# Performance work log

Measured on AMD Instinct MI355X. Metric: run time of the kernel, lower is better.

Reference implementation:

```python
import jax, jax.numpy as jnp
import numpy as np

N_NODES = 50000
N_EDGES = 800000
HEADS = 6
LEAKY = 0.2


def gat_layer(x, W, a_src, a_dst, src, dst):
    """Multi-head GAT layer (Velickovic et al.), concat heads + ELU.
    x: [N, F_in], W: [H, F_in, F_out], a_src/a_dst: [H, F_out]."""
    n = x.shape[0]
    h = jnp.einsum('nf,hfo->nho', x, W)              # [N, H, F_out]
    es = jnp.einsum('nho,ho->nh', h, a_src)          # source attention term
    ed = jnp.einsum('nho,ho->nh', h, a_dst)          # destination attention term
    e = jax.nn.leaky_relu(es[src] + ed[dst], LEAKY)  # [E, H] per-edge logits
    # segment softmax over incoming edges of each destination node
    emax = jax.ops.segment_max(e, dst, num_segments=n)
    emax = jnp.where(jnp.isfinite(emax), emax, jnp.zeros_like(emax))
    ex = jnp.exp(e - emax[dst])                      # [E, H]
    denom = jax.ops.segment_sum(ex, dst, num_segments=n)
    alpha = ex / (denom[dst] + 1e-16)                # [E, H]
    msg = alpha[:, :, None] * h[src]                 # [E, H, F_out]
    out = jax.ops.segment_sum(msg, dst, num_segments=n)  # [N, H, F_out]
    return jax.nn.elu(out).reshape(n, -1)            # concat heads


def setup_inputs() -> dict:
    key = jax.random.key(0)
    ks = jax.random.split(key, 16)
    glorot = lambda k, shape: jax.random.normal(k, shape, jnp.float32) * np.sqrt(2.0 / (shape[-2] + shape[-1]))
    inp = {
        'x': jax.random.normal(ks[0], (N_NODES, 11), jnp.float32),
        'edge_index': jax.random.randint(ks[1], (2, N_EDGES), 0, N_NODES, jnp.int32),
        'W1': glorot(ks[2], (HEADS, 11, 16)),
        'a1s': glorot(ks[3], (HEADS, 16)),
        'a1d': glorot(ks[4], (HEADS, 16)),
        'W2': glorot(ks[5], (HEADS, 96, 32)),
        'a2s': glorot(ks[6], (HEADS, 32)),
        'a2d': glorot(ks[7], (HEADS, 32)),
        'W3': glorot(ks[8], (HEADS, 192, 64)),
        'a3s': glorot(ks[9], (HEADS, 64)),
        'a3d': glorot(ks[10], (HEADS, 64)),
        'Wd': glorot(ks[11], (384, 1)),
        'bd': jnp.zeros((1,), jnp.float32),
    }
    return inp


def reference(x, edge_index, W1, a1s, a1d, W2, a2s, a2d, W3, a3s, a3d, Wd, bd):
    src, dst = edge_index[0], edge_index[1]
    h = gat_layer(x, W1, a1s, a1d, src, dst)   # [N, 96]
    h = gat_layer(h, W2, a2s, a2d, src, dst)   # [N, 192]
    h = gat_layer(h, W3, a3s, a3d, src, dst)   # [N, 384]
    g = jnp.sum(h, axis=0).reshape(1, -1)      # sum pool -> [1, 384]
    g = g / jnp.maximum(jnp.linalg.norm(g, axis=1, keepdims=True), 1e-12)  # F.normalize
    out = g @ Wd + bd                          # Dense 384->1, linear nonlin
    return jnp.squeeze(out, 1)                 # [1]
```

## Files before the change

### kernel.cpp

```cpp
#include <hip/hip_runtime.h>
#include <hip/hip_bf16.h>


#define HHEADS 6

typedef __attribute__((ext_vector_type(8))) short bf16x8;
typedef __attribute__((ext_vector_type(4))) float f32x4;
typedef __attribute__((ext_vector_type(2))) float f32x2;

typedef __attribute__((address_space(3))) unsigned int lds_uint;
typedef const __attribute__((address_space(1))) unsigned int glb_uint;

__device__ __forceinline__ float bfl(unsigned u) { return __uint_as_float(u << 16); }
__device__ __forceinline__ float bfh(unsigned u) { return __uint_as_float(u & 0xffff0000u); }
__device__ __forceinline__ unsigned short f2bf(float v) {
    unsigned u = __float_as_uint(v);
    return (unsigned short)((u + 0x7fffu + ((u >> 16) & 1u)) >> 16);
}
__device__ __forceinline__ float bf2f(unsigned short h) {
    return __uint_as_float((unsigned)h << 16);
}
__device__ __forceinline__ unsigned fkey(float f) {
    unsigned u = __float_as_uint(f);
    return (u >> 31) ? ~u : (u | 0x80000000u);
}
__device__ __forceinline__ float funkey(unsigned k) {
    return (k >> 31) ? __uint_as_float(k & 0x7fffffffu) : __uint_as_float(~k);
}

__device__ __forceinline__ void xpose4(float& v0, float& v1, float& v2, float& v3, int b) {
    bool hi = (b & 2) != 0;
    float s0 = hi ? v0 : v2;
    float s1 = hi ? v1 : v3;
    s0 = __shfl_xor(s0, 2, 64);
    s1 = __shfl_xor(s1, 2, 64);
    v0 = hi ? s0 : v0;
    v1 = hi ? s1 : v1;
    v2 = hi ? v2 : s0;
    v3 = hi ? v3 : s1;
    bool od = (b & 1) != 0;
    float t0 = od ? v0 : v1;
    t0 = __shfl_xor(t0, 1, 64);
    v0 = od ? t0 : v0;
    v1 = od ? v1 : t0;
    float t1 = od ? v2 : v3;
    t1 = __shfl_xor(t1, 1, 64);
    v2 = od ? t1 : v2;
    v3 = od ? v3 : t1;
}

__global__ void zero_misc(int* __restrict__ count, int* __restrict__ cursor,
                          float* __restrict__ g, unsigned* __restrict__ gmax,
                          unsigned short* __restrict__ apH,
                          long pad3_off, long pad3_cnt, long pad6_off, long pad6_cnt, int n) {
    long i = (long)blockIdx.x * blockDim.x + threadIdx.x;
    long stride = (long)gridDim.x * blockDim.x;
    for (long j = i; j < n; j += stride) {
        count[j] = 0;
        cursor[j] = 0;
    }
    if (i < 384) g[i] = 0.f;
    if (i < 12) gmax[i] = 0u;
    for (long j = i; j < pad3_cnt; j += stride) apH[pad3_off + j] = 0;
    for (long j = i; j < pad6_cnt; j += stride) apH[pad6_off + j] = 0;
}

__global__ void hist_kernel(const int* __restrict__ dst, int* __restrict__ count, int E) {
    int e = blockIdx.x * blockDim.x + threadIdx.x;
    if (e >= E) return;
    atomicAdd(&count[dst[e]], 1);
}

__global__ void scan_block(const int* __restrict__ count, int* __restrict__ offsets,
                           int* __restrict__ bsum, int n) {
    __shared__ int s[1024];
    int i = blockIdx.x * 1024 + threadIdx.x;
    int v = (i < n) ? count[i] : 0;
    s[threadIdx.x] = v;
    __syncthreads();
    for (int off = 1; off < 1024; off <<= 1) {
        int t = (threadIdx.x >= (unsigned)off) ? s[threadIdx.x - off] : 0;
        __syncthreads();
        s[threadIdx.x] += t;
        __syncthreads();
    }
    if (i < n) offsets[i] = s[threadIdx.x] - v;
    if (threadIdx.x == 1023) bsum[blockIdx.x] = s[1023];
}

__global__ void scan_tops(int* __restrict__ bsum, int nb) {
    __shared__ int s[64];
    int t = threadIdx.x;
    int v = (t < nb) ? bsum[t] : 0;
    s[t] = v;
    __syncthreads();
    for (int off = 1; off < 64; off <<= 1) {
        int tmp = (t >= off) ? s[t - off] : 0;
        __syncthreads();
        s[t] += tmp;
        __syncthreads();
    }
    if (t < nb) bsum[t] = s[t] - v;
}

__global__ void scan_add(int* __restrict__ offsets, const int* __restrict__ bsum, int n,
                         int total) {
    int i = blockIdx.x * 1024 + threadIdx.x;
    if (i < n) offsets[i] += bsum[blockIdx.x];
    if (i == 0) offsets[n] = total;
}

__global__ void scatter_kernel(const int* __restrict__ src, const int* __restrict__ dst,
                               const int* __restrict__ offsets, int* __restrict__ cursor,
                               int* __restrict__ ssrc, int E) {
    int e = blockIdx.x * blockDim.x + threadIdx.x;
    if (e >= E) return;
    int d = dst[e];
    int pos = offsets[d] + atomicAdd(&cursor[d], 1);
    ssrc[pos] = src[e];
}

__global__ void repack_w(const float* __restrict__ W, float* __restrict__ Wp, int FIN, int F) {
    int HF = HHEADS * F;
    int i = blockIdx.x * blockDim.x + threadIdx.x;
    if (i >= FIN * HF) return;
    int k = i / HF, c = i % HF;
    int hd = c / F, f = c % F;
    Wp[i] = W[(hd * FIN + k) * F + f];
}

__global__ void repack_w_mfma(const float* __restrict__ W, unsigned short* __restrict__ bh,
                              int FIN, int F, int NPAD) {
    int i = blockIdx.x * blockDim.x + threadIdx.x;
    if (i >= FIN * NPAD) return;
    int k = i / NPAD, n = i % NPAD;
    int NKT = FIN / 32;
    int HF = HHEADS * F;
    float w = 0.f;
    if (n < HF) {
        int hd = n / F, f = n % F;
        w = W[(hd * FIN + k) * F + f];
    }
    size_t e = ((size_t)((n >> 4) * NKT + (k >> 5)) * 64 + ((n & 15) | (((k >> 3) & 3) << 4))) * 8 +
               (k & 7);
    bh[e] = f2bf(w);
}

template <int BM, int BN, int BK>
__global__ __launch_bounds__(256) void gemm_small_attn(const float* __restrict__ A,
                                                       const float* __restrict__ B,
                                                       unsigned char* __restrict__ C8,
                                                       const float* __restrict__ as_,
                                                       const float* __restrict__ ad_,
                                                       float* __restrict__ es,
                                                       float* __restrict__ ed, int M, int K,
                                                       int N) {
    __shared__ float As[BK][BM + 4];
    __shared__ float Bs[BK][BN];
    int tid = threadIdx.x;
    int tx = tid % 16, ty = tid / 16;
    int m0 = blockIdx.y * BM, n0 = blockIdx.x * BN;
    float acc[4][4] = {};
    for (int kk0 = 0; kk0 < K; kk0 += BK) {
#pragma unroll
        for (int i = 0; i < (BM * BK) / 256; ++i) {
            int idx = tid + i * 256;
            int m = idx / BK, k = idx % BK;
            float v = 0.f;
            if (m0 + m < M && kk0 + k < K) v = A[(size_t)(m0 + m) * K + kk0 + k];
            As[k][m] = v;
        }
#pragma unroll
        for (int i = 0; i < (BK * BN) / 1024; ++i) {
            int idx = tid + i * 256;
            int k = idx / (BN / 4), n4 = idx % (BN / 4);
            float4 v = make_float4(0.f, 0.f, 0.f, 0.f);
            if (kk0 + k < K && n0 + n4 * 4 < N)
                v = *(const float4*)&B[(size_t)(kk0 + k) * N + n0 + n4 * 4];
            *(float4*)&Bs[k][n4 * 4] = v;
        }
        __syncthreads();
#pragma unroll
        for (int k = 0; k < BK; ++k) {
            float4 av = *(const float4*)&As[k][ty * 4];
            float4 bv = *(const float4*)&Bs[k][tx * 4];
            float a[4] = {av.x, av.y, av.z, av.w};
            float b[4] = {bv.x, bv.y, bv.z, bv.w};
#pragma unroll
            for (int i = 0; i < 4; ++i)
#pragma unroll
                for (int j = 0; j < 4; ++j) acc[i][j] += a[i] * b[j];
        }
        __syncthreads();
    }
    bool colok = (n0 + tx * 4) < N;
    float asv[4], adv[4];
#pragma unroll
    for (int j = 0; j < 4; ++j) {
        int col = n0 + tx * 4 + j;
        asv[j] = (col < N) ? as_[col] : 0.f;
        adv[j] = (col < N) ? ad_[col] : 0.f;
    }
#pragma unroll
    for (int i = 0; i < 4; ++i) {
        int m = m0 + ty * 4 + i;
        bool mok = m < M;
        if (mok && colok) {
            int pk = __builtin_amdgcn_cvt_pk_fp8_f32(acc[i][0], acc[i][1], 0, false);
            pk = __builtin_amdgcn_cvt_pk_fp8_f32(acc[i][2], acc[i][3], pk, true);
            *(unsigned*)&C8[(size_t)m * N + n0 + tx * 4] = (unsigned)pk;
        }
        float ps = 0.f, pd = 0.f;
#pragma unroll
        for (int j = 0; j < 4; ++j) {
            ps += acc[i][j] * asv[j];
            pd += acc[i][j] * adv[j];
        }
        ps += __shfl_down(ps, 2, 4);
        ps += __shfl_down(ps, 1, 4);
        pd += __shfl_down(pd, 2, 4);
        pd += __shfl_down(pd, 1, 4);
        if (mok && colok && (tx & 3) == 0) {
            int hd = (n0 + tx * 4) >> 4;
            es[(size_t)m * HHEADS + hd] = ps;
            ed[(size_t)m * HHEADS + hd] = pd;
        }
    }
}

template <int K, int NREAL, int NPAD, int F, int MT>
__global__ __launch_bounds__(256) void gemm_attn_mfma(
    const unsigned short* __restrict__ Ah, const unsigned short* __restrict__ Bh,
    unsigned char* __restrict__ C8, const float* __restrict__ as_,
    const float* __restrict__ ad_, float* __restrict__ es, float* __restrict__ ed,
    unsigned* __restrict__ gmax, int M) {
    constexpr int NKT = K / 32;
    __shared__ unsigned short sB[NKT * 4096];
    __shared__ unsigned short sA[2][4096];
    int tid = threadIdx.x;
    int lane = tid & 63, wave = tid >> 6;
    int wrow = wave >> 1, wcol = wave & 1;
    int quad = lane >> 4, c16 = lane & 15;

    int nwg = gridDim.x * gridDim.y;
    int hh = blockIdx.y * gridDim.x + blockIdx.x;
    int q = nwg >> 3, r = nwg & 7;
    int xcd = hh & 7, pos = hh >> 3;
    int wk = (xcd < r ? xcd * (q + 1) : r * (q + 1) + (xcd - r) * q) + pos;
    int bx = wk % gridDim.x, by = wk / gridDim.x;

    int n0 = bx * 128;
    int bn16 = n0 >> 4;
    int nmt = (M + 127) >> 7;

#pragma unroll
    for (int kt2 = 0; kt2 < NKT; ++kt2) {
#pragma unroll
        for (int rep = 0; rep < 2; ++rep) {
            int chunk = tid + rep * 256;
            int tile = chunk >> 6, e8 = chunk & 63;
            size_t boff = ((size_t)((bn16 + tile) * NKT + kt2) * 64 + e8) * 8;
            __builtin_amdgcn_global_load_lds((glb_uint*)&Bh[boff],
                                             (lds_uint*)&sB[kt2 * 4096 + chunk * 8], 16, 0, 0);
        }
    }
    auto STAGE_A = [&](int mti, int kt2, int buf) {
#pragma unroll
        for (int rep = 0; rep < 2; ++rep) {
            int chunk = tid + rep * 256;
            int tile = chunk >> 6, e8 = chunk & 63;
            size_t aoff = ((size_t)((mti * 8 + tile) * NKT + kt2) * 64 + e8) * 8;
            __builtin_amdgcn_global_load_lds((glb_uint*)&Ah[aoff],
                                             (lds_uint*)&sA[buf][chunk * 8], 16, 0, 0);
        }
    };
    STAGE_A(min(by * MT, nmt - 1), 0, 0);
    asm volatile("s_waitcnt vmcnt(0)" ::: "memory");
    __builtin_amdgcn_s_barrier();

    float asv[4], adv[4];
#pragma unroll
    for (int j = 0; j < 4; ++j) {
        int col = n0 + wcol * 64 + j * 16 + c16;
        bool ok = col < NREAL;
        asv[j] = ok ? as_[col] : 0.f;
        adv[j] = ok ? ad_[col] : 0.f;
    }
    float mx = -1e30f;
    float mxA = -1e30f, mxB = -1e30f;
    bool colvalid = (n0 + wcol * 64) < NREAL;
    int b4 = lane & 3;

    f32x4 acc[4][4] = {};
    const int T = MT * NKT;
    int mt = 0, kt = 0;
    for (int t = 0; t < T; ++t) {
        int cur = t & 1;
        int nkt = kt + 1, nmt2 = mt;
        if (nkt == NKT) {
            nkt = 0;
            nmt2 = mt + 1;
        }
        if (t + 1 < T) STAGE_A(min(by * MT + nmt2, nmt - 1), nkt, cur ^ 1);
        bf16x8 fah[4], fbh[4];
#pragma unroll
        for (int i = 0; i < 4; ++i) {
            fah[i] = *(const bf16x8*)&sA[cur][(wrow * 4 + i) * 512 + lane * 8];
            fbh[i] = *(const bf16x8*)&sB[kt * 4096 + (wcol * 4 + i) * 512 + lane * 8];
        }
        asm volatile("s_waitcnt lgkmcnt(0)" ::: "memory");
        __builtin_amdgcn_sched_barrier(0);
#pragma unroll
        for (int i = 0; i < 4; ++i)
#pragma unroll
            for (int j = 0; j < 4; ++j)
                acc[i][j] = __builtin_amdgcn_mfma_f32_16x16x32_bf16(fah[i], fbh[j], acc[i][j],
                                                                    0, 0, 0);
        if (kt == NKT - 1) {
            int m0 = (by * MT + mt) * 128;
            if (m0 < M) {
#pragma unroll
                for (int i = 0; i < 4; ++i) {
#pragma unroll
                    for (int r2 = 0; r2 < 4; ++r2) {
                        int m = m0 + wrow * 64 + i * 16 + quad * 4 + r2;
                        bool mok = m < M;
                        if (F == 64) {
                            float ps = acc[i][0][r2] * asv[0] + acc[i][1][r2] * asv[1] +
                                       acc[i][2][r2] * asv[2] + acc[i][3][r2] * asv[3];
                            float pd = acc[i][0][r2] * adv[0] + acc[i][1][r2] * adv[1] +
                                       acc[i][2][r2] * adv[2] + acc[i][3][r2] * adv[3];
#pragma unroll
                            for (int off = 8; off > 0; off >>= 1) {
                                ps += __shfl_down(ps, off, 16);
                                pd += __shfl_down(pd, off, 16);
                            }
                            if (mok && c16 == 0) {
                                int hd = (n0 + wcol * 64) / 64;
                                es[(size_t)m * HHEADS + hd] = ps;
                                ed[(size_t)m * HHEADS + hd] = pd;
                                mx = fmaxf(mx, ps);
                            }
                        } else {
                            float psA = acc[i][0][r2] * asv[0] + acc[i][1][r2] * asv[1];
                            float pdA = acc[i][0][r2] * adv[0] + acc[i][1][r2] * adv[1];
                            float psB = acc[i][2][r2] * asv[2] + acc[i][3][r2] * asv[3];
                            float pdB = acc[i][2][r2] * adv[2] + acc[i][3][r2] * adv[3];
#pragma unroll
                            for (int off = 8; off > 0; off >>= 1) {
                                psA += __shfl_down(psA, off, 16);
                                pdA += __shfl_down(pdA, off, 16);
                                psB += __shfl_down(psB, off, 16);
                                pdB += __shfl_down(pdB, off, 16);
                            }
                            if (mok && c16 == 0 && colvalid) {
                                int colbase = n0 + wcol * 64;
                                int hd = colbase / 32;
                                es[(size_t)m * HHEADS + hd] = psA;
                                ed[(size_t)m * HHEADS + hd] = pdA;
                                es[(size_t)m * HHEADS + hd + 1] = psB;
                                ed[(size_t)m * HHEADS + hd + 1] = pdB;
                                mxA = fmaxf(mxA, psA);
                                mxB = fmaxf(mxB, psB);
                            }
                        }
                    }
                }
#pragma unroll
                for (int i = 0; i < 4; ++i) {
                    int m = m0 + wrow * 64 + i * 16 + quad * 4 + b4;
                    bool mok = m < M;
#pragma unroll
                    for (int j = 0; j < 4; ++j) {
                        float v0 = acc[i][j][0], v1 = acc[i][j][1], v2 = acc[i][j][2],
                              v3 = acc[i][j][3];
                        xpose4(v0, v1, v2, v3, b4);
                        int colb = n0 + wcol * 64 + j * 16 + (c16 & 12);
                        if (mok && (F == 64 || colvalid)) {
                            int pk = __builtin_amdgcn_cvt_pk_fp8_f32(v0, v1, 0, false);
                            pk = __builtin_amdgcn_cvt_pk_fp8_f32(v2, v3, pk, true);
                            *(unsigned*)&C8[(size_t)m * NREAL + colb] = (unsigned)pk;
                        }
                    }
                }
            }
#pragma unroll
            for (int i = 0; i < 4; ++i)
#pragma unroll
                for (int j = 0; j < 4; ++j) acc[i][j] = (f32x4){0.f, 0.f, 0.f, 0.f};
        }
        asm volatile("s_waitcnt vmcnt(0)" ::: "memory");
        __builtin_amdgcn_s_barrier();
        kt = nkt;
        mt = nmt2;
    }

    if (F == 64) {
#pragma unroll
        for (int off = 32; off > 0; off >>= 1) mx = fmaxf(mx, __shfl_xor(mx, off));
        if (lane == 0) atomicMax(&gmax[(n0 + wcol * 64) / 64], fkey(mx));
    } else {
        mxA = fmaxf(mxA, __shfl_xor(mxA, 16));
        mxA = fmaxf(mxA, __shfl_xor(mxA, 32));
        mxB = fmaxf(mxB, __shfl_xor(mxB, 16));
        mxB = fmaxf(mxB, __shfl_xor(mxB, 32));
        if (lane == 0 && colvalid) {
            int hd = (n0 + wcol * 64) / 32;
            atomicMax(&gmax[6 + hd], fkey(mxA));
            atomicMax(&gmax[6 + hd + 1], fkey(mxB));
        }
    }
}

template <int F>
__global__ __launch_bounds__(256) void aggregate_fused(
    const unsigned char* __restrict__ h8, const float* __restrict__ es,
    const float* __restrict__ ed, const int* __restrict__ offsets,
    const int* __restrict__ ssrc, unsigned short* __restrict__ oh, int n) {
    constexpr int HF = HHEADS * F;
    constexpr int C8 = HF / 8;
    int tid = blockIdx.x * blockDim.x + threadIdx.x;
    if (tid >= n * C8) return;
    int node = tid / C8, q = tid % C8;
    int c = q * 8, hd = c / F;
    int a = offsets[node], b = offsets[node + 1];
    float edv = ed[node * HHEADS + hd];
    float m = -1e30f, l = 0.f;
    float acc[8] = {};
    for (int j = a; j < b; ++j) {
        int s = ssrc[j];
        float v = es[s * HHEADS + hd] + edv;
        v = v > 0.f ? v : 0.2f * v;
        float mn = fmaxf(m, v);
        float r = __expf(m - mn);
        float wgt = __expf(v - mn);
        uint2 hv = *(const uint2*)&h8[(size_t)s * HF + c];
        f32x2 p0 = __builtin_amdgcn_cvt_pk_f32_fp8((int)hv.x, false);
        f32x2 p1 = __builtin_amdgcn_cvt_pk_f32_fp8((int)hv.x, true);
        f32x2 p2 = __builtin_amdgcn_cvt_pk_f32_fp8((int)hv.y, false);
        f32x2 p3 = __builtin_amdgcn_cvt_pk_f32_fp8((int)hv.y, true);
        l = l * r + wgt;
        acc[0] = acc[0] * r + wgt * p0[0];
        acc[1] = acc[1] * r + wgt * p0[1];
        acc[2] = acc[2] * r + wgt * p1[0];
        acc[3] = acc[3] * r + wgt * p1[1];
        acc[4] = acc[4] * r + wgt * p2[0];
        acc[5] = acc[5] * r + wgt * p2[1];
        acc[6] = acc[6] * r + wgt * p3[0];
        acc[7] = acc[7] * r + wgt * p3[1];
        m = mn;
    }
    float invd = 1.0f / (l + 1e-16f);
    unsigned short th[8];
#pragma unroll
    for (int k = 0; k < 8; ++k) {
        float v = acc[k] * invd;
        v = v > 0.f ? v : (__expf(v) - 1.0f);
        th[k] = f2bf(v);
    }
    constexpr int NKT = HF / 32;
    int lq = (node & 15) | (((c >> 3) & 3) << 4);
    size_t base = ((size_t)((node >> 4) * NKT + (c >> 5)) * 64 + lq) * 8;
    *(uint4*)&oh[base] = *(uint4*)th;
}

__global__ __launch_bounds__(256) void aggregate_wpn2(
    const unsigned char* __restrict__ h8, const float* __restrict__ es,
    const float* __restrict__ ed, const unsigned* __restrict__ gmax,
    const int* __restrict__ offsets, const int* __restrict__ ssrc,
    unsigned short* __restrict__ oh, int n) {
    constexpr int HF = 192;
    int wid = (int)((blockIdx.x * (unsigned)blockDim.x + threadIdx.x) >> 6);
    int lane = threadIdx.x & 63;
    if (wid >= n || lane >= 48) return;
    int node = wid;
    int hd = lane >> 3;
    int c = lane * 4;
    int a = offsets[node], b = offsets[node + 1];
    float edv = ed[node * HHEADS + hd];
    float mv = funkey(gmax[6 + hd]) + edv;
    float m = mv > 0.f ? mv : 0.2f * mv;
    float l = 0.f;
    float acc[4] = {};
    const unsigned char* hbase = h8 + c;
    int j = a;
    for (; j + 1 < b; j += 2) {
        int s0 = ssrc[j], s1 = ssrc[j + 1];
        float ev0 = es[(size_t)s0 * HHEADS + hd];
        float ev1 = es[(size_t)s1 * HHEADS + hd];
        unsigned h0 = *(const unsigned*)(hbase + (size_t)s0 * HF);
        unsigned h1 = *(const unsigned*)(hbase + (size_t)s1 * HF);
        float v0 = ev0 + edv;
        v0 = v0 > 0.f ? v0 : 0.2f * v0;
        float v1 = ev1 + edv;
        v1 = v1 > 0.f ? v1 : 0.2f * v1;
        float w0 = __expf(v0 - m);
        float w1 = __expf(v1 - m);
        {
            f32x2 p0 = __builtin_amdgcn_cvt_pk_f32_fp8((int)h0, false);
            f32x2 p1 = __builtin_amdgcn_cvt_pk_f32_fp8((int)h0, true);
            l += w0;
            acc[0] += w0 * p0[0];
            acc[1] += w0 * p0[1];
            acc[2] += w0 * p1[0];
            acc[3] += w0 * p1[1];
        }
        {
            f32x2 p0 = __builtin_amdgcn_cvt_pk_f32_fp8((int)h1, false);
            f32x2 p1 = __builtin_amdgcn_cvt_pk_f32_fp8((int)h1, true);
            l += w1;
            acc[0] += w1 * p0[0];
            acc[1] += w1 * p0[1];
            acc[2] += w1 * p1[0];
            acc[3] += w1 * p1[1];
        }
    }
    if (j < b) {
        int s0 = ssrc[j];
        float ev0 = es[(size_t)s0 * HHEADS + hd];
        unsigned h0 = *(const unsigned*)(hbase + (size_t)s0 * HF);
        float v0 = ev0 + edv;
        v0 = v0 > 0.f ? v0 : 0.2f * v0;
        float w0 = __expf(v0 - m);
        f32x2 p0 = __builtin_amdgcn_cvt_pk_f32_fp8((int)h0, false);
        f32x2 p1 = __builtin_amdgcn_cvt_pk_f32_fp8((int)h0, true);
        l += w0;
        acc[0] += w0 * p0[0];
        acc[1] += w0 * p0[1];
        acc[2] += w0 * p1[0];
        acc[3] += w0 * p1[1];
    }
    float invd = 1.0f / (l + 1e-16f);
    unsigned short th[4];
#pragma unroll
    for (int k = 0; k < 4; ++k) {
        float v = acc[k] * invd;
        v = v > 0.f ? v : (__expf(v) - 1.0f);
        th[k] = f2bf(v);
    }
    int lq = (node & 15) | (((c >> 3) & 3) << 4);
    size_t base = ((size_t)((node >> 4) * (HF / 32) + (c >> 5)) * 64 + lq) * 8 + (c & 7);
    *(uint2*)&oh[base] = *(uint2*)th;
}

__global__ __launch_bounds__(256) void aggregate_wpn3(
    const unsigned char* __restrict__ h8, const float* __restrict__ es,
    const float* __restrict__ ed, const unsigned* __restrict__ gmax,
    const int* __restrict__ offsets, const int* __restrict__ ssrc,
    __hip_bfloat16* __restrict__ outb, int n) {
    constexpr int HF = 384;
    int wid = (int)((blockIdx.x * (unsigned)blockDim.x + threadIdx.x) >> 6);
    int lane = threadIdx.x & 63;
    if (wid >= n || lane >= 48) return;
    int node = wid;
    int hd = lane >> 3;
    int c = lane * 8;
    int a = offsets[node], b = offsets[node + 1];
    float edv = ed[node * HHEADS + hd];
    float mv = funkey(gmax[hd]) + edv;
    float m = mv > 0.f ? mv : 0.2f * mv;
    float l = 0.f;
    float acc[8] = {};
    const unsigned char* hbase = h8 + c;
    int j = a;
    for (; j + 1 < b; j += 2) {
        int s0 = ssrc[j], s1 = ssrc[j + 1];
        float ev0 = es[(size_t)s0 * HHEADS + hd];
        float ev1 = es[(size_t)s1 * HHEADS + hd];
        uint2 h0 = *(const uint2*)(hbase + (size_t)s0 * HF);
        uint2 h1 = *(const uint2*)(hbase + (size_t)s1 * HF);
        float v0 = ev0 + edv;
        v0 = v0 > 0.f ? v0 : 0.2f * v0;
        float v1 = ev1 + edv;
        v1 = v1 > 0.f ? v1 : 0.2f * v1;
        float w0 = __expf(v0 - m);
        float w1 = __expf(v1 - m);
        {
            f32x2 p0 = __builtin_amdgcn_cvt_pk_f32_fp8((int)h0.x, false);
            f32x2 p1 = __builtin_amdgcn_cvt_pk_f32_fp8((int)h0.x, true);
            f32x2 p2 = __builtin_amdgcn_cvt_pk_f32_fp8((int)h0.y, false);
            f32x2 p3 = __builtin_amdgcn_cvt_pk_f32_fp8((int)h0.y, true);
            l += w0;
            acc[0] += w0 * p0[0];
            acc[1] += w0 * p0[1];
            acc[2] += w0 * p1[0];
            acc[3] += w0 * p1[1];
            acc[4] += w0 * p2[0];
            acc[5] += w0 * p2[1];
            acc[6] += w0 * p3[0];
            acc[7] += w0 * p3[1];
        }
        {
            f32x2 p0 = __builtin_amdgcn_cvt_pk_f32_fp8((int)h1.x, false);
            f32x2 p1 = __builtin_amdgcn_cvt_pk_f32_fp8((int)h1.x, true);
            f32x2 p2 = __builtin_amdgcn_cvt_pk_f32_fp8((int)h1.y, false);
            f32x2 p3 = __builtin_amdgcn_cvt_pk_f32_fp8((int)h1.y, true);
            l += w1;
            acc[0] += w1 * p0[0];
            acc[1] += w1 * p0[1];
            acc[2] += w1 * p1[0];
            acc[3] += w1 * p1[1];
            acc[4] += w1 * p2[0];
            acc[5] += w1 * p2[1];
            acc[6] += w1 * p3[0];
            acc[7] += w1 * p3[1];
        }
    }
    if (j < b) {
        int s0 = ssrc[j];
        float ev0 = es[(size_t)s0 * HHEADS + hd];
        uint2 h0 = *(const uint2*)(hbase + (size_t)s0 * HF);
        float v0 = ev0 + edv;
        v0 = v0 > 0.f ? v0 : 0.2f * v0;
        float w0 = __expf(v0 - m);
        f32x2 p0 = __builtin_amdgcn_cvt_pk_f32_fp8((int)h0.x, false);
        f32x2 p1 = __builtin_amdgcn_cvt_pk_f32_fp8((int)h0.x, true);
        f32x2 p2 = __builtin_amdgcn_cvt_pk_f32_fp8((int)h0.y, false);
        f32x2 p3 = __builtin_amdgcn_cvt_pk_f32_fp8((int)h0.y, true);
        l += w0;
        acc[0] += w0 * p0[0];
        acc[1] += w0 * p0[1];
        acc[2] += w0 * p1[0];
        acc[3] += w0 * p1[1];
        acc[4] += w0 * p2[0];
        acc[5] += w0 * p2[1];
        acc[6] += w0 * p3[0];
        acc[7] += w0 * p3[1];
    }
    float invd = 1.0f / (l + 1e-16f);
    __hip_bfloat16 tb[8];
#pragma unroll
    for (int k = 0; k < 8; ++k) {
        float v = acc[k] * invd;
        v = v > 0.f ? v : (__expf(v) - 1.0f);
        tb[k] = __float2bfloat16(v);
    }
    *(uint4*)&outb[(size_t)node * HF + c] = *(uint4*)tb;
}

__global__ void pool_kernel(const __hip_bfloat16* __restrict__ out3, float* __restrict__ g,
                            int n) {
    int b = blockIdx.x, t = threadIdx.x;
    int chunk = (n + gridDim.x - 1) / gridDim.x;
    int n0 = b * chunk, n1 = min(n, n0 + chunk);
    float a0 = 0.f, a1 = 0.f;
    const unsigned* p = (const unsigned*)out3;
    for (int node = n0; node < n1; ++node) {
        unsigned u = p[(size_t)node * 192 + t];
        a0 += bfl(u);
        a1 += bfh(u);
    }
    atomicAdd(&g[2 * t], a0);
    atomicAdd(&g[2 * t + 1], a1);
}

__global__ void final_kernel(const float* __restrict__ g, const float* __restrict__ Wd,
                             const float* __restrict__ bd, float* __restrict__ outp) {
    __shared__ float red[384];
    int t = threadIdx.x;
    float v = g[t];
    red[t] = v * v;
    __syncthreads();
    for (int s = 192; s >= 3; s >>= 1) {
        if (t < s) red[t] += red[t + s];
        __syncthreads();
    }
    __shared__ float scale_s;
    if (t == 0) {
        float norm = sqrtf(red[0] + red[1] + red[2]);
        scale_s = 1.0f / fmaxf(norm, 1e-12f);
    }
    __syncthreads();
    float scale = scale_s;
    red[t] = v * scale * Wd[t];
    __syncthreads();
    for (int s = 192; s >= 3; s >>= 1) {
        if (t < s) red[t] += red[t + s];
        __syncthreads();
    }
    if (t == 0) outp[0] = red[0] + red[1] + red[2] + bd[0];
}

extern "C" void kernel_launch(void* const* d_in, const int* in_sizes, int n_in, void* d_out,
                              int out_size, void* d_ws, size_t ws_size, hipStream_t stream) {
    const float* x = (const float*)d_in[0];
    const int* ei = (const int*)d_in[1];
    const float* W1 = (const float*)d_in[2];
    const float* a1s = (const float*)d_in[3];
    const float* a1d = (const float*)d_in[4];
    const float* W2 = (const float*)d_in[5];
    const float* a2s = (const float*)d_in[6];
    const float* a2d = (const float*)d_in[7];
    const float* W3 = (const float*)d_in[8];
    const float* a3s = (const float*)d_in[9];
    const float* a3d = (const float*)d_in[10];
    const float* Wd = (const float*)d_in[11];
    const float* bd = (const float*)d_in[12];
    float* outp = (float*)d_out;

    const int N = in_sizes[0] / 11;
    const int E = in_sizes[1] / 2;
    const int* src = ei;
    const int* dst = ei + E;

    const int NT16 = ((N + 127) / 128) * 8;
    const int NMT = (N + 127) / 128;

    char* w = (char*)d_ws;
    size_t off = 0;
    auto A = [&](size_t bytes) {
        size_t o = off;
        off += (bytes + 255) & ~(size_t)255;
        return o;
    };
    unsigned char* bufH = (unsigned char*)(w + A((size_t)N * 384 * 2));
    __hip_bfloat16* bufO = (__hip_bfloat16*)(w + A((size_t)N * 384 * 2));
    unsigned short* apH = (unsigned short*)(w + A((size_t)NT16 * 6 * 512 * 2));
    unsigned short* b2H = (unsigned short*)(w + A((size_t)16 * 3 * 512 * 2));
    unsigned short* b3H = (unsigned short*)(w + A((size_t)24 * 6 * 512 * 2));
    float* es = (float*)(w + A((size_t)N * HHEADS * 4));
    float* ed = (float*)(w + A((size_t)N * HHEADS * 4));
    unsigned* gmax = (unsigned*)(w + A(256));
    float* wp = (float*)(w + A((size_t)11 * 96 * 4));
    int* count = (int*)(w + A((size_t)(N + 1) * 4));
    int* cursor = (int*)(w + A((size_t)(N + 1) * 4));
    int* offsets = (int*)(w + A((size_t)(N + 1) * 4));
    int* bsum = (int*)(w + A(64 * 4));
    int* ssrc = (int*)(w + A((size_t)E * 4));
    float* g = (float*)(w + A(384 * 4));

    const long t16v = N / 16;
    const long padT = NT16 - t16v;
    zero_misc<<<(N + 255) / 256, 256, 0, stream>>>(count, cursor, g, gmax, apH,
                                                   t16v * 3 * 512, padT * 3 * 512,
                                                   t16v * 6 * 512, padT * 6 * 512, N);

    hist_kernel<<<(E + 255) / 256, 256, 0, stream>>>(dst, count, E);
    int nb = (N + 1023) / 1024;
    scan_block<<<nb, 1024, 0, stream>>>(count, offsets, bsum, N);
    scan_tops<<<1, 64, 0, stream>>>(bsum, nb);
    scan_add<<<nb, 1024, 0, stream>>>(offsets, bsum, N, E);
    scatter_kernel<<<(E + 255) / 256, 256, 0, stream>>>(src, dst, offsets, cursor, ssrc, E);

    repack_w<<<(11 * 96 + 255) / 256, 256, 0, stream>>>(W1, wp, 11, 16);
    repack_w_mfma<<<(96 * 256 + 255) / 256, 256, 0, stream>>>(W2, b2H, 96, 32, 256);
    repack_w_mfma<<<(192 * 384 + 255) / 256, 256, 0, stream>>>(W3, b3H, 192, 64, 384);

    {
        dim3 grid((96 + 63) / 64, (N + 63) / 64);
        gemm_small_attn<64, 64, 32><<<grid, 256, 0, stream>>>(x, wp, bufH, a1s, a1d, es, ed, N,
                                                              11, 96);
    }
    {
        long total = (long)N * (96 / 8);
        aggregate_fused<16><<<(total + 255) / 256, 256, 0, stream>>>(bufH, es, ed, offsets,
                                                                     ssrc, apH, N);
    }

    {
        dim3 grid(2, (NMT + 3) / 4);
        gemm_attn_mfma<96, 192, 256, 32, 4><<<grid, 256, 0, stream>>>(apH, b2H, bufH, a2s,
                                                                      a2d, es, ed, gmax, N);
    }
    {
        int grid = (N + 3) / 4;
        aggregate_wpn2<<<grid, 256, 0, stream>>>(bufH, es, ed, gmax, offsets, ssrc, apH, N);
    }

    {
        dim3 grid(3, (NMT + 3) / 4);
        gemm_attn_mfma<192, 384, 384, 64, 4><<<grid, 256, 0, stream>>>(apH, b3H, bufH, a3s,
                                                                       a3d, es, ed, gmax, N);
    }
    {
        int grid = (N + 3) / 4;
        aggregate_wpn3<<<grid, 256, 0, stream>>>(bufH, es, ed, gmax, offsets, ssrc, bufO, N);
    }

    pool_kernel<<<256, 192, 0, stream>>>(bufO, g, N);
    final_kernel<<<1, 384, 0, stream>>>(g, Wd, bd, outp);
}
```

Before: 513.3 us.

## Slice layer-3 fp8 features into 48-byte column slabs for cache-local aggregation

The layer-3 GEMM now writes its fp8 output as eight column slices of 48 bytes per node, each stored contiguously across all nodes. A new slice-major aggregation kernel has each block work within one slice, so the gathered source rows of a slice stay in a smaller working set that fits better in cache. This replaces the wave-per-node kernel that read the full 384-byte rows. Accumulations in all aggregation kernels are also rewritten with packed f32x2 vectors so the compiler can emit packed FMA. The costs are that every edge's index and attention score are now re-read once per slice, and the 2-way edge unroll in the layer-3 loop is dropped.

Result: slower. 564.5 us (+10.0%).

```diff
diff --git a/kernel.cpp b/kernel.cpp
--- a/kernel.cpp
+++ b/kernel.cpp
@@ -379,7 +379,13 @@
                         if (mok && (F == 64 || colvalid)) {
                             int pk = __builtin_amdgcn_cvt_pk_fp8_f32(v0, v1, 0, false);
                             pk = __builtin_amdgcn_cvt_pk_fp8_f32(v2, v3, pk, true);
-                            *(unsigned*)&C8[(size_t)m * NREAL + colb] = (unsigned)pk;
+                            if (F == 64) {
+                                int sl = colb / 48, of = colb - sl * 48;
+                                *(unsigned*)&C8[(size_t)sl * ((size_t)M * 48) +
+                                                (size_t)m * 48 + of] = (unsigned)pk;
+                            } else {
+                                *(unsigned*)&C8[(size_t)m * NREAL + colb] = (unsigned)pk;
+                            }
                         }
                     }
                 }
@@ -426,7 +432,7 @@
     int a = offsets[node], b = offsets[node + 1];
     float edv = ed[node * HHEADS + hd];
     float m = -1e30f, l = 0.f;
-    float acc[8] = {};
+    f32x2 a0 = {0.f, 0.f}, a1 = {0.f, 0.f}, a2 = {0.f, 0.f}, a3 = {0.f, 0.f};
     for (int j = a; j < b; ++j) {
         int s = ssrc[j];
         float v = es[s * HHEADS + hd] + edv;
@@ -440,21 +446,19 @@
         f32x2 p2 = __builtin_amdgcn_cvt_pk_f32_fp8((int)hv.y, false);
         f32x2 p3 = __builtin_amdgcn_cvt_pk_f32_fp8((int)hv.y, true);
         l = l * r + wgt;
-        acc[0] = acc[0] * r + wgt * p0[0];
-        acc[1] = acc[1] * r + wgt * p0[1];
-        acc[2] = acc[2] * r + wgt * p1[0];
-        acc[3] = acc[3] * r + wgt * p1[1];
-        acc[4] = acc[4] * r + wgt * p2[0];
-        acc[5] = acc[5] * r + wgt * p2[1];
-        acc[6] = acc[6] * r + wgt * p3[0];
-        acc[7] = acc[7] * r + wgt * p3[1];
+        f32x2 rv = {r, r}, wv = {wgt, wgt};
+        a0 = a0 * rv + wv * p0;
+        a1 = a1 * rv + wv * p1;
+        a2 = a2 * rv + wv * p2;
+        a3 = a3 * rv + wv * p3;
         m = mn;
     }
     float invd = 1.0f / (l + 1e-16f);
+    float res[8] = {a0[0], a0[1], a1[0], a1[1], a2[0], a2[1], a3[0], a3[1]};
     unsigned short th[8];
 #pragma unroll
     for (int k = 0; k < 8; ++k) {
-        float v = acc[k] * invd;
+        float v = res[k] * invd;
         v = v > 0.f ? v : (__expf(v) - 1.0f);
         th[k] = f2bf(v);
     }
@@ -481,7 +485,7 @@
     float mv = funkey(gmax[6 + hd]) + edv;
     float m = mv > 0.f ? mv : 0.2f * mv;
     float l = 0.f;
-    float acc[4] = {};
+    f32x2 a0 = {0.f, 0.f}, a1 = {0.f, 0.f};
     const unsigned char* hbase = h8 + c;
     int j = a;
     for (; j + 1 < b; j += 2) {
@@ -499,20 +503,18 @@
         {
             f32x2 p0 = __builtin_amdgcn_cvt_pk_f32_fp8((int)h0, false);
             f32x2 p1 = __builtin_amdgcn_cvt_pk_f32_fp8((int)h0, true);
+            f32x2 wv = {w0, w0};
             l += w0;
-            acc[0] += w0 * p0[0];
-            acc[1] += w0 * p0[1];
-            acc[2] += w0 * p1[0];
-            acc[3] += w0 * p1[1];
+            a0 = a0 + wv * p0;
+            a1 = a1 + wv * p1;
         }
         {
             f32x2 p0 = __builtin_amdgcn_cvt_pk_f32_fp8((int)h1, false);
             f32x2 p1 = __builtin_amdgcn_cvt_pk_f32_fp8((int)h1, true);
+            f32x2 wv = {w1, w1};
             l += w1;
-            acc[0] += w1 * p0[0];
-            acc[1] += w1 * p0[1];
-            acc[2] += w1 * p1[0];
-            acc[3] += w1 * p1[1];
+            a0 = a0 + wv * p0;
+            a1 = a1 + wv * p1;
         }
     }
     if (j < b) {
@@ -524,17 +526,17 @@
         float w0 = __expf(v0 - m);
         f32x2 p0 = __builtin_amdgcn_cvt_pk_f32_fp8((int)h0, false);
         f32x2 p1 = __builtin_amdgcn_cvt_pk_f32_fp8((int)h0, true);
+        f32x2 wv = {w0, w0};
         l += w0;
-        acc[0] += w0 * p0[0];
-        acc[1] += w0 * p0[1];
-        acc[2] += w0 * p1[0];
-        acc[3] += w0 * p1[1];
+        a0 = a0 + wv * p0;
+        a1 = a1 + wv * p1;
     }
     float invd = 1.0f / (l + 1e-16f);
+    float res[4] = {a0[0], a0[1], a1[0], a1[1]};
     unsigned short th[4];
 #pragma unroll
     for (int k = 0; k < 4; ++k) {
-        float v = acc[k] * invd;
+        float v = res[k] * invd;
         v = v > 0.f ? v : (__expf(v) - 1.0f);
         th[k] = f2bf(v);
     }
@@ -543,99 +545,51 @@
     *(uint2*)&oh[base] = *(uint2*)th;
 }
 
-__global__ __launch_bounds__(256) void aggregate_wpn3(
-    const unsigned char* __restrict__ h8, const float* __restrict__ es,
+__global__ __launch_bounds__(256) void aggregate_sp3(
+    const unsigned char* __restrict__ hs, const float* __restrict__ es,
     const float* __restrict__ ed, const unsigned* __restrict__ gmax,
     const int* __restrict__ offsets, const int* __restrict__ ssrc,
     __hip_bfloat16* __restrict__ outb, int n) {
-    constexpr int HF = 384;
-    int wid = (int)((blockIdx.x * (unsigned)blockDim.x + threadIdx.x) >> 6);
-    int lane = threadIdx.x & 63;
-    if (wid >= n || lane >= 48) return;
-    int node = wid;
-    int hd = lane >> 3;
-    int c = lane * 8;
+    int sl = blockIdx.x & 7;
+    long gt = (long)(blockIdx.x >> 3) * 256 + threadIdx.x;
+    if (gt >= (long)n * 6) return;
+    int node = (int)(gt / 6), q = (int)(gt % 6);
+    int cbase = sl * 48 + q * 8;
+    int hd = cbase >> 6;
     int a = offsets[node], b = offsets[node + 1];
     float edv = ed[node * HHEADS + hd];
     float mv = funkey(gmax[hd]) + edv;
     float m = mv > 0.f ? mv : 0.2f * mv;
     float l = 0.f;
-    float acc[8] = {};
-    const unsigned char* hbase = h8 + c;
-    int j = a;
-    for (; j + 1 < b; j += 2) {
-        int s0 = ssrc[j], s1 = ssrc[j + 1];
-        float ev0 = es[(size_t)s0 * HHEADS + hd];
-        float ev1 = es[(size_t)s1 * HHEADS + hd];
-        uint2 h0 = *(const uint2*)(hbase + (size_t)s0 * HF);
-        uint2 h1 = *(const uint2*)(hbase + (size_t)s1 * HF);
-        float v0 = ev0 + edv;
-        v0 = v0 > 0.f ? v0 : 0.2f * v0;
-        float v1 = ev1 + edv;
-        v1 = v1 > 0.f ? v1 : 0.2f * v1;
-        float w0 = __expf(v0 - m);
-        float w1 = __expf(v1 - m);
-        {
-            f32x2 p0 = __builtin_amdgcn_cvt_pk_f32_fp8((int)h0.x, false);
-            f32x2 p1 = __builtin_amdgcn_cvt_pk_f32_fp8((int)h0.x, true);
-            f32x2 p2 = __builtin_amdgcn_cvt_pk_f32_fp8((int)h0.y, false);
-            f32x2 p3 = __builtin_amdgcn_cvt_pk_f32_fp8((int)h0.y, true);
-            l += w0;
-            acc[0] += w0 * p0[0];
-            acc[1] += w0 * p0[1];
-            acc[2] += w0 * p1[0];
-            acc[3] += w0 * p1[1];
-            acc[4] += w0 * p2[0];
-            acc[5] += w0 * p2[1];
-            acc[6] += w0 * p3[0];
-            acc[7] += w0 * p3[1];
-        }
-        {
-            f32x2 p0 = __builtin_amdgcn_cvt_pk_f32_fp8((int)h1.x, false);
-            f32x2 p1 = __builtin_amdgcn_cvt_pk_f32_fp8((int)h1.x, true);
-            f32x2 p2 = __builtin_amdgcn_cvt_pk_f32_fp8((int)h1.y, false);
-            f32x2 p3 = __builtin_amdgcn_cvt_pk_f32_fp8((int)h1.y, true);
-            l += w1;
-            acc[0] += w1 * p0[0];
-            acc[1] += w1 * p0[1];
-            acc[2] += w1 * p1[0];
-            acc[3] += w1 * p1[1];
-            acc[4] += w1 * p2[0];
-            acc[5] += w1 * p2[1];
-            acc[6] += w1 * p3[0];
-            acc[7] += w1 * p3[1];
-        }
-    }
-    if (j < b) {
-        int s0 = ssrc[j];
-        float ev0 = es[(size_t)s0 * HHEADS + hd];
-        uint2 h0 = *(const uint2*)(hbase + (size_t)s0 * HF);
-        float v0 = ev0 + edv;
-        v0 = v0 > 0.f ? v0 : 0.2f * v0;
-        float w0 = __expf(v0 - m);
-        f32x2 p0 = __builtin_amdgcn_cvt_pk_f32_fp8((int)h0.x, false);
-        f32x2 p1 = __builtin_amdgcn_cvt_pk_f32_fp8((int)h0.x, true);
-        f32x2 p2 = __builtin_amdgcn_cvt_pk_f32_fp8((int)h0.y, false);
-        f32x2 p3 = __builtin_amdgcn_cvt_pk_f32_fp8((int)h0.y, true);
-        l += w0;
-        acc[0] += w0 * p0[0];
-        acc[1] += w0 * p0[1];
-        acc[2] += w0 * p1[0];
-        acc[3] += w0 * p1[1];
-        acc[4] += w0 * p2[0];
-        acc[5] += w0 * p2[1];
-        acc[6] += w0 * p3[0];
-        acc[7] += w0 * p3[1];
+    f32x2 a0 = {0.f, 0.f}, a1 = {0.f, 0.f}, a2 = {0.f, 0.f}, a3 = {0.f, 0.f};
+    const unsigned char* base = hs + (size_t)sl * ((size_t)n * 48) + q * 8;
+    for (int j = a; j < b; ++j) {
+        int s = ssrc[j];
+        float v = es[(size_t)s * HHEADS + hd] + edv;
+        v = v > 0.f ? v : 0.2f * v;
+        float w = __expf(v - m);
+        uint2 hv = *(const uint2*)(base + (size_t)s * 48);
+        f32x2 p0 = __builtin_amdgcn_cvt_pk_f32_fp8((int)hv.x, false);
+        f32x2 p1 = __builtin_amdgcn_cvt_pk_f32_fp8((int)hv.x, true);
+        f32x2 p2 = __builtin_amdgcn_cvt_pk_f32_fp8((int)hv.y, false);
+        f32x2 p3 = __builtin_amdgcn_cvt_pk_f32_fp8((int)hv.y, true);
+        f32x2 wv = {w, w};
+        l += w;
+        a0 = a0 + wv * p0;
+        a1 = a1 + wv * p1;
+        a2 = a2 + wv * p2;
+        a3 = a3 + wv * p3;
     }
     float invd = 1.0f / (l + 1e-16f);
+    float res[8] = {a0[0], a0[1], a1[0], a1[1], a2[0], a2[1], a3[0], a3[1]};
     __hip_bfloat16 tb[8];
 #pragma unroll
     for (int k = 0; k < 8; ++k) {
-        float v = acc[k] * invd;
+        float v = res[k] * invd;
         v = v > 0.f ? v : (__expf(v) - 1.0f);
         tb[k] = __float2bfloat16(v);
     }
-    *(uint4*)&outb[(size_t)node * HF + c] = *(uint4*)tb;
+    *(uint4*)&outb[(size_t)node * 384 + cbase] = *(uint4*)tb;
 }
 
 __global__ void pool_kernel(const __hip_bfloat16* __restrict__ out3, float* __restrict__ g,
@@ -773,8 +727,9 @@
                                                                        a3d, es, ed, gmax, N);
     }
     {
-        int grid = (N + 3) / 4;
-        aggregate_wpn3<<<grid, 256, 0, stream>>>(bufH, es, ed, gmax, offsets, ssrc, bufO, N);
+        long groups = ((long)N * 6 + 255) / 256;
+        aggregate_sp3<<<(int)(groups * 8), 256, 0, stream>>>(bufH, es, ed, gmax, offsets,
+                                                             ssrc, bufO, N);
     }
 
     pool_kernel<<<256, 192, 0, stream>>>(bufO, g, N);
```
